# Optimization experiments

Measured on AMD Instinct MI355X. Metric: run time of the kernel, lower is better.

Reference implementation:

```python
import jax, jax.numpy as jnp
import numpy as np

B, NODES, IN_DIM, OUT_DIM, CAPS, K, NUM_ROUTE = 32, 512, 256, 128, 16, 5, 3

def squash(s):
    # s: [..., out]; scale = |s|^2/(1+|s|^2), direction s/(|s|+eps)
    sn = jnp.sum(s * s, axis=-1, keepdims=True)
    return (sn / (1.0 + sn)) * s / (jnp.sqrt(sn) + 1e-8)

def setup_inputs() -> dict:
    key = jax.random.key(0)
    k1, k2, k3, k4 = jax.random.split(key, 4)
    return {
        "x": jax.random.normal(k1, (B, NODES, IN_DIM), jnp.float32),
        "contribution": jax.random.normal(k2, (B, NODES), jnp.float32),
        "W": jax.random.normal(k3, (K, IN_DIM, OUT_DIM), jnp.float32),
        "alpha": jax.random.normal(k4, (NODES, CAPS, K), jnp.float32),
    }

def reference(x, contribution, W, alpha):
    # per-node, per-capsule transform: sum_k alpha[n,c,k] * W[k,i,o] -> [nodes, caps, in, out]
    Wn = jnp.einsum('nck,kio->ncio', alpha, W)
    # prediction vectors u_hat: [B, caps, nodes, out]
    u_hat = jnp.einsum('bni,ncio->bcno', x, Wn)
    u_det = jax.lax.stop_gradient(u_hat)
    # routing logits b init from (detached) contribution: [B, caps, nodes, 1]
    b = jnp.broadcast_to(
        jax.lax.stop_gradient(contribution)[:, None, :, None],
        (x.shape[0], CAPS, x.shape[1], 1))
    for _ in range(NUM_ROUTE):
        c = jax.nn.softmax(b, axis=1)              # over capsule axis
        v = squash(jnp.sum(c * u_det, axis=2))     # [B, caps, out]
        b = b + jnp.einsum('bcno,bco->bcn', u_det, v)[..., None]
    c = jax.nn.softmax(b, axis=1)
    s = jnp.sum(c * u_hat, axis=2)                 # [B, caps, out] (non-detached)
    return squash(s)
```

## Files before the change

kernel.cpp:

```cpp
#include <hip/hip_runtime.h>
#include <math.h>

#define B_ 32
#define NODES_ 512
#define IN_ 256
#define OUT_ 128
#define CAPS_ 16
#define KW_ 5
#define M_ (B_*NODES_)
#define N_ (KW_*OUT_)
#define NCH 32

typedef __attribute__((ext_vector_type(8))) short short8;
typedef __attribute__((ext_vector_type(4))) float f32x4;

#define Y_BOFF   0
#define L_BOFF   41943040
#define V_BOFF   42991616
#define SP_BOFF  43253760
#define BT_SZ    (N_*IN_*2)

__device__ __forceinline__ float b2f(unsigned short u) {
  union { unsigned int i; float f; } c; c.i = ((unsigned int)u) << 16; return c.f;
}

__device__ __forceinline__ unsigned short f2b(float f) {
  union { float f; unsigned int i; } c; c.f = f;
  unsigned int u = c.i;
  u += 0x7fffu + ((u >> 16) & 1u);
  return (unsigned short)(u >> 16);
}

__device__ __forceinline__ void async_load16(const void* g, void* l) {
  __builtin_amdgcn_global_load_lds(
      (const __attribute__((address_space(1))) unsigned int*)g,
      (__attribute__((address_space(3))) unsigned int*)l, 16, 0, 0);
}

__global__ __launch_bounds__(256) void conv_w(const float* __restrict__ W,
                                              unsigned short* __restrict__ bThi,
                                              unsigned short* __restrict__ bTlo) {
  int n = blockIdx.x;
  int i = threadIdx.x;
  int k = n >> 7, o = n & 127;
  float v = W[((size_t)k*IN_ + i)*OUT_ + o];
  unsigned short h = f2b(v);
  bThi[(size_t)n*IN_ + i] = h;
  bTlo[(size_t)n*IN_ + i] = f2b(v - b2f(h));
}

__global__ __launch_bounds__(256) void gemm_mfma(const float* __restrict__ x,
                                                 const unsigned short* __restrict__ bThi,
                                                 const unsigned short* __restrict__ bTlo,
                                                 float* __restrict__ y) {
  __shared__ float A_lds[8*128*4];
  __shared__ short Bh_lds[4*128*8];
  __shared__ short Bl_lds[4*128*8];
  const int t    = threadIdx.x;
  const int w    = t >> 6;
  const int lane = t & 63;
  const int wm   = w >> 1;
  const int wn   = w & 1;
  const int m0   = blockIdx.x * 128;
  const int n0   = blockIdx.y * 128;
  const int lrow = lane & 15;
  const int lk   = lane >> 4;

  f32x4 acc[4][4];
  #pragma unroll
  for (int i=0;i<4;++i)
    #pragma unroll
    for (int j=0;j<4;++j) acc[i][j] = (f32x4){0.f,0.f,0.f,0.f};

  for (int kb = 0; kb < IN_; kb += 32) {
    #pragma unroll
    for (int q=0; q<4; ++q) {
      int d0 = q*256 + w*64;
      int d  = d0 + lane;
      int cg = d >> 7;
      int r  = d & 127;
      async_load16(x + (size_t)(m0 + r)*IN_ + kb + cg*4, &A_lds[d0*4]);
    }
    #pragma unroll
    for (int q=0; q<2; ++q) {
      int d0 = q*256 + w*64;
      int d  = d0 + lane;
      int cg = d >> 7;
      int r  = d & 127;
      async_load16(bThi + (size_t)(n0 + r)*IN_ + kb + cg*8, &Bh_lds[d0*8]);
      async_load16(bTlo + (size_t)(n0 + r)*IN_ + kb + cg*8, &Bl_lds[d0*8]);
    }
    __syncthreads();

    short8 ah[4], al[4], bh[4], bl[4];
    #pragma unroll
    for (int mi=0; mi<4; ++mi) {
      int row_a = wm*64 + mi*16 + lrow;
      f32x4 a0 = *(const f32x4*)&A_lds[((2*lk  )*128 + row_a)*4];
      f32x4 a1 = *(const f32x4*)&A_lds[((2*lk+1)*128 + row_a)*4];
      #pragma unroll
      for (int j=0; j<8; ++j) {
        float f = (j < 4) ? a0[j] : a1[j-4];
        unsigned short h = f2b(f);
        ah[mi][j] = (short)h;
        al[mi][j] = (short)f2b(f - b2f(h));
      }
    }
    #pragma unroll
    for (int ni=0; ni<4; ++ni) {
      int row_b = wn*64 + ni*16 + lrow;
      bh[ni] = *(const short8*)&Bh_lds[(lk*128 + row_b)*8];
      bl[ni] = *(const short8*)&Bl_lds[(lk*128 + row_b)*8];
    }
    #pragma unroll
    for (int mi=0; mi<4; ++mi)
      #pragma unroll
      for (int ni=0; ni<4; ++ni) {
        acc[mi][ni] = __builtin_amdgcn_mfma_f32_16x16x32_bf16(bh[ni], ah[mi], acc[mi][ni], 0, 0, 0);
        acc[mi][ni] = __builtin_amdgcn_mfma_f32_16x16x32_bf16(bh[ni], al[mi], acc[mi][ni], 0, 0, 0);
        acc[mi][ni] = __builtin_amdgcn_mfma_f32_16x16x32_bf16(bl[ni], ah[mi], acc[mi][ni], 0, 0, 0);
      }
    __syncthreads();
  }

  #pragma unroll
  for (int mi=0; mi<4; ++mi) {
    int m = m0 + wm*64 + mi*16 + lrow;
    #pragma unroll
    for (int ni=0; ni<4; ++ni) {
      int nb = n0 + wn*64 + ni*16 + lk*4;
      float4 o = {acc[mi][ni][0], acc[mi][ni][1], acc[mi][ni][2], acc[mi][ni][3]};
      *(float4*)(y + (size_t)m*N_ + nb) = o;
    }
  }
}

__global__ __launch_bounds__(256) void route_step(const float* __restrict__ y,
                                                  const float* __restrict__ alpha,
                                                  const float* __restrict__ contrib,
                                                  float* __restrict__ logits,
                                                  const float* __restrict__ vin,
                                                  float* __restrict__ s_part,
                                                  int mode) {
  __shared__ __align__(16) float sh_y[16*644];
  __shared__ __align__(16) float sh_v[16*132];
  __shared__ __align__(16) float sh_alpha[16*16*5];
  __shared__ float sh_logit[16][16];
  __shared__ float sh_cw[16][16];

  const int t  = threadIdx.x;
  const int ch = blockIdx.x;
  const int b  = blockIdx.y;
  const int n0 = ch*16;

  const float* ybase = y + ((size_t)(b*NODES_ + n0))*KW_*OUT_;
  #pragma unroll
  for (int q=0; q<10; ++q) {
    int idx4 = t + q*256;
    int flat = idx4*4;
    int node = flat / 640;
    int rem  = flat - node*640;
    float4 vv = *(const float4*)(ybase + flat);
    *(float4*)&sh_y[node*644 + rem] = vv;
  }
  const float* abase = alpha + (size_t)n0*CAPS_*KW_;
  for (int i = t; i < 320; i += 256) {
    float4 av = *(const float4*)(abase + i*4);
    *(float4*)&sh_alpha[i*4] = av;
  }
  if (mode >= 1) {
    const float* vbase = vin + (size_t)b*CAPS_*OUT_;
    #pragma unroll
    for (int q=0; q<2; ++q) {
      int flat = (t + q*256)*4;
      int c = flat >> 7, o = flat & 127;
      float4 vv = *(const float4*)(vbase + flat);
      *(float4*)&sh_v[c*132 + o] = vv;
    }
    int node = t & 15, cap = t >> 4;
    sh_logit[node][cap] = logits[((size_t)b*CAPS_ + cap)*NODES_ + n0 + node];
  } else {
    int node = t & 15, cap = t >> 4;
    float cv = contrib[(size_t)b*NODES_ + n0 + node];
    sh_logit[node][cap] = cv;
    logits[((size_t)b*CAPS_ + cap)*NODES_ + n0 + node] = cv;
  }
  __syncthreads();

  if (mode >= 1) {
    int node = t >> 4, cap = t & 15;
    const float* al = &sh_alpha[(node*16+cap)*5];
    float a0=al[0],a1=al[1],a2=al[2],a3=al[3],a4=al[4];
    const float* yb = &sh_y[node*644];
    const float* vb = &sh_v[cap*132];
    float accd = 0.f;
    #pragma unroll 4
    for (int o=0; o<128; o+=4) {
      float4 y0 = *(const float4*)(yb + 0*128 + o);
      float4 y1 = *(const float4*)(yb + 1*128 + o);
      float4 y2 = *(const float4*)(yb + 2*128 + o);
      float4 y3 = *(const float4*)(yb + 3*128 + o);
      float4 y4 = *(const float4*)(yb + 4*128 + o);
      float4 vv = *(const float4*)(vb + o);
      float ux = a0*y0.x + a1*y1.x + a2*y2.x + a3*y3.x + a4*y4.x;
      float uy = a0*y0.y + a1*y1.y + a2*y2.y + a3*y3.y + a4*y4.y;
      float uz = a0*y0.z + a1*y1.z + a2*y2.z + a3*y3.z + a4*y4.z;
      float uw = a0*y0.w + a1*y1.w + a2*y2.w + a3*y3.w + a4*y4.w;
      accd += ux*vv.x + uy*vv.y + uz*vv.z + uw*vv.w;
    }
    float newl = sh_logit[node][cap] + accd;
    sh_logit[node][cap] = newl;
    logits[((size_t)b*CAPS_ + cap)*NODES_ + n0 + node] = newl;
    __syncthreads();
    if (t < 16) {
      int nd = t;
      float m = -1e30f;
      #pragma unroll
      for (int c=0;c<16;++c) m = fmaxf(m, sh_logit[nd][c]);
      float s = 0.f;
      float e[16];
      #pragma unroll
      for (int c=0;c<16;++c) { e[c] = __expf(sh_logit[nd][c]-m); s += e[c]; }
      float inv = 1.f/s;
      #pragma unroll
      for (int c=0;c<16;++c) sh_cw[nd][c] = e[c]*inv;
    }
  } else {
    int node = t >> 4, cap = t & 15;
    sh_cw[node][cap] = 1.f/16.f;
  }
  __syncthreads();

  float* spb = s_part + ((size_t)(b*NCH + ch))*CAPS_*OUT_;
  #pragma unroll
  for (int sl=0; sl<2; ++sl) {
    int slot = t + sl*256;
    int c = slot >> 5;
    int o = (slot & 31) * 4;
    float4 acc = {0.f,0.f,0.f,0.f};
    #pragma unroll 4
    for (int nd=0; nd<16; ++nd) {
      const float* al = &sh_alpha[(nd*16+c)*5];
      float a0=al[0],a1=al[1],a2=al[2],a3=al[3],a4=al[4];
      const float* yb = &sh_y[nd*644 + o];
      float4 y0 = *(const float4*)(yb);
      float4 y1 = *(const float4*)(yb + 128);
      float4 y2 = *(const float4*)(yb + 256);
      float4 y3 = *(const float4*)(yb + 384);
      float4 y4 = *(const float4*)(yb + 512);
      float cw = sh_cw[nd][c];
      acc.x += cw*(a0*y0.x + a1*y1.x + a2*y2.x + a3*y3.x + a4*y4.x);
      acc.y += cw*(a0*y0.y + a1*y1.y + a2*y2.y + a3*y3.y + a4*y4.y);
      acc.z += cw*(a0*y0.z + a1*y1.z + a2*y2.z + a3*y3.z + a4*y4.z);
      acc.w += cw*(a0*y0.w + a1*y1.w + a2*y2.w + a3*y3.w + a4*y4.w);
    }
    *(float4*)(spb + c*OUT_ + o) = acc;
  }
}

__global__ __launch_bounds__(128) void squash_k(const float* __restrict__ s_part,
                                                float* __restrict__ out) {
  const int bc = blockIdx.x;
  const int o  = threadIdx.x;
  const int b = bc >> 4, c = bc & 15;
  const float* sp = s_part + ((size_t)(b*NCH)*CAPS_ + c)*OUT_ + o;
  float s = 0.f;
  #pragma unroll
  for (int ch=0; ch<NCH; ++ch) s += sp[(size_t)ch*CAPS_*OUT_];
  float ss = s*s;
  #pragma unroll
  for (int off=32; off>0; off>>=1) ss += __shfl_down(ss, off, 64);
  __shared__ float red[2];
  if ((o & 63) == 0) red[o>>6] = ss;
  __syncthreads();
  float sn = red[0] + red[1];
  float scale = (sn/(1.f+sn)) / (sqrtf(sn)+1e-8f);
  out[(size_t)bc*OUT_ + o] = scale*s;
}

extern "C" void kernel_launch(void* const* d_in, const int* in_sizes, int n_in,
                              void* d_out, int out_size, void* d_ws, size_t ws_size,
                              hipStream_t stream) {
  const float* x       = (const float*)d_in[0];
  const float* contrib = (const float*)d_in[1];
  const float* W       = (const float*)d_in[2];
  const float* alpha   = (const float*)d_in[3];
  float* out = (float*)d_out;
  char*  wsb = (char*)d_ws;

  float* y             = (float*)(wsb + Y_BOFF);
  float* logits        = (float*)(wsb + L_BOFF);
  float* v             = (float*)(wsb + V_BOFF);
  float* s_part        = (float*)(wsb + SP_BOFF);
  unsigned short* bThi = (unsigned short*)(wsb + SP_BOFF);
  unsigned short* bTlo = (unsigned short*)(wsb + SP_BOFF + BT_SZ);

  conv_w<<<N_, 256, 0, stream>>>(W, bThi, bTlo);
  gemm_mfma<<<dim3(M_/128, N_/128), 256, 0, stream>>>(x, bThi, bTlo, y);

  route_step<<<dim3(NCH, B_), 256, 0, stream>>>(y, alpha, contrib, logits, v, s_part, 0);
  squash_k<<<B_*CAPS_, 128, 0, stream>>>(s_part, v);

  for (int it=0; it<3; ++it) {
    route_step<<<dim3(NCH, B_), 256, 0, stream>>>(y, alpha, contrib, logits, v, s_part, 1);
    squash_k<<<B_*CAPS_, 128, 0, stream>>>(s_part, (it==2) ? out : v);
  }
}
```

Baseline: 153.4 us.

## Pre-split x to bf16 hi/lo, use smaller GEMM tiles and 8-node routing chunks

Adds a conv_x pass that splits x into bf16 hi/lo arrays once, so the GEMM streams pre-split bf16 A tiles through async LDS loads instead of converting fp32 x inside the kernel. The GEMM tile shrinks to 64 rows with launch bounds asking for 4 blocks per CU, and the routing kernel handles 8 nodes per block across 64 chunks, giving more blocks and less LDS per block. The squash reduction is templated on the chunk count. The new path runs only when the workspace is large enough, otherwise the old path is kept. It costs an extra pass over x and twice as many partial sums to reduce.

Result: slower. 232.9 us (+51.8%).

```diff
diff --git a/kernel.cpp b/kernel.cpp
--- a/kernel.cpp
+++ b/kernel.cpp
@@ -9,7 +9,6 @@
 #define KW_ 5
 #define M_ (B_*NODES_)
 #define N_ (KW_*OUT_)
-#define NCH 32
 
 typedef __attribute__((ext_vector_type(8))) short short8;
 typedef __attribute__((ext_vector_type(4))) float f32x4;
@@ -19,22 +18,37 @@
 #define V_BOFF   42991616
 #define SP_BOFF  43253760
 #define BT_SZ    (N_*IN_*2)
+#define SP64_SZ  (B_*64*CAPS_*OUT_*4)
+#define WS_NEED_BIG (SP_BOFF + SP64_SZ)
+#define XSP_SZ   (M_*IN_*2)
 
 __device__ __forceinline__ float b2f(unsigned short u) {
   union { unsigned int i; float f; } c; c.i = ((unsigned int)u) << 16; return c.f;
 }
-
 __device__ __forceinline__ unsigned short f2b(float f) {
   union { float f; unsigned int i; } c; c.f = f;
   unsigned int u = c.i;
   u += 0x7fffu + ((u >> 16) & 1u);
   return (unsigned short)(u >> 16);
 }
-
 __device__ __forceinline__ void async_load16(const void* g, void* l) {
   __builtin_amdgcn_global_load_lds(
       (const __attribute__((address_space(1))) unsigned int*)g,
       (__attribute__((address_space(3))) unsigned int*)l, 16, 0, 0);
+}
+
+__global__ __launch_bounds__(256) void conv_x(const float* __restrict__ x,
+                                              unsigned short* __restrict__ xhi,
+                                              unsigned short* __restrict__ xlo) {
+  int idx = blockIdx.x*256 + threadIdx.x;
+  float4 v = *(const float4*)(x + (size_t)idx*4);
+  ushort4 h, l;
+  h.x = f2b(v.x); l.x = f2b(v.x - b2f(h.x));
+  h.y = f2b(v.y); l.y = f2b(v.y - b2f(h.y));
+  h.z = f2b(v.z); l.z = f2b(v.z - b2f(h.z));
+  h.w = f2b(v.w); l.w = f2b(v.w - b2f(h.w));
+  *(ushort4*)(xhi + (size_t)idx*4) = h;
+  *(ushort4*)(xlo + (size_t)idx*4) = l;
 }
 
 __global__ __launch_bounds__(256) void conv_w(const float* __restrict__ W,
@@ -49,10 +63,84 @@
   bTlo[(size_t)n*IN_ + i] = f2b(v - b2f(h));
 }
 
-__global__ __launch_bounds__(256) void gemm_mfma(const float* __restrict__ x,
-                                                 const unsigned short* __restrict__ bThi,
-                                                 const unsigned short* __restrict__ bTlo,
-                                                 float* __restrict__ y) {
+__global__ __launch_bounds__(256, 4) void gemm_bf4(const unsigned short* __restrict__ xhi,
+                                                   const unsigned short* __restrict__ xlo,
+                                                   const unsigned short* __restrict__ bThi,
+                                                   const unsigned short* __restrict__ bTlo,
+                                                   float* __restrict__ y) {
+  __shared__ short Ah_lds[4*64*8];
+  __shared__ short Al_lds[4*64*8];
+  __shared__ short Bh_lds[4*128*8];
+  __shared__ short Bl_lds[4*128*8];
+  const int t    = threadIdx.x;
+  const int lane = t & 63;
+  const int w    = t >> 6;
+  const int wm   = w >> 1;
+  const int wn   = w & 1;
+  const int m0   = blockIdx.x * 64;
+  const int n0   = blockIdx.y * 128;
+  const int lrow = lane & 15;
+  const int lk   = lane >> 4;
+
+  f32x4 acc[2][4];
+  #pragma unroll
+  for (int i=0;i<2;++i)
+    #pragma unroll
+    for (int j=0;j<4;++j) acc[i][j] = (f32x4){0.f,0.f,0.f,0.f};
+
+  const int cgA = t >> 6, rA = t & 63;
+  for (int kb = 0; kb < IN_; kb += 32) {
+    async_load16(xhi + (size_t)(m0 + rA)*IN_ + kb + cgA*8, &Ah_lds[t*8]);
+    async_load16(xlo + (size_t)(m0 + rA)*IN_ + kb + cgA*8, &Al_lds[t*8]);
+    #pragma unroll
+    for (int q=0; q<2; ++q) {
+      int d  = q*256 + t;
+      int cg = d >> 7, r = d & 127;
+      async_load16(bThi + (size_t)(n0 + r)*IN_ + kb + cg*8, &Bh_lds[d*8]);
+      async_load16(bTlo + (size_t)(n0 + r)*IN_ + kb + cg*8, &Bl_lds[d*8]);
+    }
+    __syncthreads();
+
+    short8 ah[2], al[2], bh[4], bl[4];
+    #pragma unroll
+    for (int mi=0; mi<2; ++mi) {
+      int row_a = wm*32 + mi*16 + lrow;
+      ah[mi] = *(const short8*)&Ah_lds[(lk*64 + row_a)*8];
+      al[mi] = *(const short8*)&Al_lds[(lk*64 + row_a)*8];
+    }
+    #pragma unroll
+    for (int ni=0; ni<4; ++ni) {
+      int row_b = wn*64 + ni*16 + lrow;
+      bh[ni] = *(const short8*)&Bh_lds[(lk*128 + row_b)*8];
+      bl[ni] = *(const short8*)&Bl_lds[(lk*128 + row_b)*8];
+    }
+    #pragma unroll
+    for (int mi=0; mi<2; ++mi)
+      #pragma unroll
+      for (int ni=0; ni<4; ++ni) {
+        acc[mi][ni] = __builtin_amdgcn_mfma_f32_16x16x32_bf16(bh[ni], ah[mi], acc[mi][ni], 0, 0, 0);
+        acc[mi][ni] = __builtin_amdgcn_mfma_f32_16x16x32_bf16(bh[ni], al[mi], acc[mi][ni], 0, 0, 0);
+        acc[mi][ni] = __builtin_amdgcn_mfma_f32_16x16x32_bf16(bl[ni], ah[mi], acc[mi][ni], 0, 0, 0);
+      }
+    __syncthreads();
+  }
+
+  #pragma unroll
+  for (int mi=0; mi<2; ++mi) {
+    int m = m0 + wm*32 + mi*16 + lrow;
+    #pragma unroll
+    for (int ni=0; ni<4; ++ni) {
+      int nb = n0 + wn*64 + ni*16 + lk*4;
+      float4 o = {acc[mi][ni][0], acc[mi][ni][1], acc[mi][ni][2], acc[mi][ni][3]};
+      *(float4*)(y + (size_t)m*N_ + nb) = o;
+    }
+  }
+}
+
+__global__ __launch_bounds__(256) void gemm_insplit(const float* __restrict__ x,
+                                                    const unsigned short* __restrict__ bThi,
+                                                    const unsigned short* __restrict__ bTlo,
+                                                    float* __restrict__ y) {
   __shared__ float A_lds[8*128*4];
   __shared__ short Bh_lds[4*128*8];
   __shared__ short Bl_lds[4*128*8];
@@ -135,13 +223,146 @@
   }
 }
 
-__global__ __launch_bounds__(256) void route_step(const float* __restrict__ y,
-                                                  const float* __restrict__ alpha,
-                                                  const float* __restrict__ contrib,
-                                                  float* __restrict__ logits,
-                                                  const float* __restrict__ vin,
-                                                  float* __restrict__ s_part,
-                                                  int mode) {
+__global__ __launch_bounds__(256) void route_step8(const float* __restrict__ y,
+                                                   const float* __restrict__ alpha,
+                                                   const float* __restrict__ contrib,
+                                                   float* __restrict__ logits,
+                                                   const float* __restrict__ vin,
+                                                   float* __restrict__ s_part,
+                                                   int mode) {
+  __shared__ __align__(16) float sh_y[8*644];
+  __shared__ __align__(16) float sh_v[16*132];
+  __shared__ __align__(16) float sh_alpha[8*16*5];
+  __shared__ float sh_logit[8][16];
+  __shared__ float sh_cw[8][16];
+
+  const int t  = threadIdx.x;
+  const int ch = blockIdx.x;
+  const int b  = blockIdx.y;
+  const int n0 = ch*8;
+
+  const float* ybase = y + ((size_t)(b*NODES_ + n0))*KW_*OUT_;
+  #pragma unroll
+  for (int q=0; q<5; ++q) {
+    int idx4 = t + q*256;
+    int flat = idx4*4;
+    int node = flat / 640;
+    int rem  = flat - node*640;
+    float4 vv = *(const float4*)(ybase + flat);
+    *(float4*)&sh_y[node*644 + rem] = vv;
+  }
+  const float* abase = alpha + (size_t)n0*CAPS_*KW_;
+  if (t < 160) {
+    float4 av = *(const float4*)(abase + t*4);
+    *(float4*)&sh_alpha[t*4] = av;
+  }
+  if (mode >= 1) {
+    const float* vbase = vin + (size_t)b*CAPS_*OUT_;
+    #pragma unroll
+    for (int q=0; q<2; ++q) {
+      int flat = (t + q*256)*4;
+      int c = flat >> 7, o = flat & 127;
+      float4 vv = *(const float4*)(vbase + flat);
+      *(float4*)&sh_v[c*132 + o] = vv;
+    }
+    if (t < 128) {
+      int node = t & 7, cap = t >> 3;
+      sh_logit[node][cap] = logits[((size_t)b*CAPS_ + cap)*NODES_ + n0 + node];
+    }
+  } else {
+    if (t < 128) {
+      int node = t & 7, cap = t >> 3;
+      float cv = contrib[(size_t)b*NODES_ + n0 + node];
+      sh_logit[node][cap] = cv;
+      logits[((size_t)b*CAPS_ + cap)*NODES_ + n0 + node] = cv;
+    }
+  }
+  __syncthreads();
+
+  if (mode >= 1) {
+    int node = t >> 5, cap = (t >> 1) & 15, half = t & 1;
+    const float* al = &sh_alpha[(node*16+cap)*5];
+    float a0=al[0],a1=al[1],a2=al[2],a3=al[3],a4=al[4];
+    const float* yb = &sh_y[node*644] + half*64;
+    const float* vb = &sh_v[cap*132]  + half*64;
+    float accd = 0.f;
+    #pragma unroll 4
+    for (int o=0; o<64; o+=4) {
+      float4 y0 = *(const float4*)(yb + 0*128 + o);
+      float4 y1 = *(const float4*)(yb + 1*128 + o);
+      float4 y2 = *(const float4*)(yb + 2*128 + o);
+      float4 y3 = *(const float4*)(yb + 3*128 + o);
+      float4 y4 = *(const float4*)(yb + 4*128 + o);
+      float4 vv = *(const float4*)(vb + o);
+      float ux = a0*y0.x + a1*y1.x + a2*y2.x + a3*y3.x + a4*y4.x;
+      float uy = a0*y0.y + a1*y1.y + a2*y2.y + a3*y3.y + a4*y4.y;
+      float uz = a0*y0.z + a1*y1.z + a2*y2.z + a3*y3.z + a4*y4.z;
+      float uw = a0*y0.w + a1*y1.w + a2*y2.w + a3*y3.w + a4*y4.w;
+      accd += ux*vv.x + uy*vv.y + uz*vv.z + uw*vv.w;
+    }
+    float tot = accd + __shfl_xor(accd, 1, 64);
+    if (half == 0) {
+      float newl = sh_logit[node][cap] + tot;
+      sh_logit[node][cap] = newl;
+      logits[((size_t)b*CAPS_ + cap)*NODES_ + n0 + node] = newl;
+    }
+    __syncthreads();
+    if (t < 8) {
+      int nd = t;
+      float m = -1e30f;
+      #pragma unroll
+      for (int c=0;c<16;++c) m = fmaxf(m, sh_logit[nd][c]);
+      float s = 0.f;
+      float e[16];
+      #pragma unroll
+      for (int c=0;c<16;++c) { e[c] = __expf(sh_logit[nd][c]-m); s += e[c]; }
+      float inv = 1.f/s;
+      #pragma unroll
+      for (int c=0;c<16;++c) sh_cw[nd][c] = e[c]*inv;
+    }
+  } else {
+    if (t < 128) sh_cw[t & 7][t >> 3] = 1.f/16.f;
+  }
+  __syncthreads();
+
+  {
+    int c  = t >> 4;
+    int o0 = (t & 15)*8;
+    float acc[8] = {0,0,0,0,0,0,0,0};
+    #pragma unroll 2
+    for (int nd=0; nd<8; ++nd) {
+      const float* al = &sh_alpha[(nd*16+c)*5];
+      float a0=al[0],a1=al[1],a2=al[2],a3=al[3],a4=al[4];
+      float cw = sh_cw[nd][c];
+      const float* yb = &sh_y[nd*644 + o0];
+      #pragma unroll
+      for (int h=0; h<2; ++h) {
+        float4 y0 = *(const float4*)(yb + h*4);
+        float4 y1 = *(const float4*)(yb + 128 + h*4);
+        float4 y2 = *(const float4*)(yb + 256 + h*4);
+        float4 y3 = *(const float4*)(yb + 384 + h*4);
+        float4 y4 = *(const float4*)(yb + 512 + h*4);
+        acc[h*4+0] += cw*(a0*y0.x + a1*y1.x + a2*y2.x + a3*y3.x + a4*y4.x);
+        acc[h*4+1] += cw*(a0*y0.y + a1*y1.y + a2*y2.y + a3*y3.y + a4*y4.y);
+        acc[h*4+2] += cw*(a0*y0.z + a1*y1.z + a2*y2.z + a3*y3.z + a4*y4.z);
+        acc[h*4+3] += cw*(a0*y0.w + a1*y1.w + a2*y2.w + a3*y3.w + a4*y4.w);
+      }
+    }
+    float* spb = s_part + ((size_t)(b*64 + ch)*CAPS_ + c)*OUT_ + o0;
+    float4 w0 = {acc[0],acc[1],acc[2],acc[3]};
+    float4 w1 = {acc[4],acc[5],acc[6],acc[7]};
+    *(float4*)(spb)     = w0;
+    *(float4*)(spb + 4) = w1;
+  }
+}
+
+__global__ __launch_bounds__(256) void route_step16(const float* __restrict__ y,
+                                                    const float* __restrict__ alpha,
+                                                    const float* __restrict__ contrib,
+                                                    float* __restrict__ logits,
+                                                    const float* __restrict__ vin,
+                                                    float* __restrict__ s_part,
+                                                    int mode) {
   __shared__ __align__(16) float sh_y[16*644];
   __shared__ __align__(16) float sh_v[16*132];
   __shared__ __align__(16) float sh_alpha[16*16*5];
@@ -231,7 +452,7 @@
   }
   __syncthreads();
 
-  float* spb = s_part + ((size_t)(b*NCH + ch))*CAPS_*OUT_;
+  float* spb = s_part + ((size_t)(b*32 + ch))*CAPS_*OUT_;
   #pragma unroll
   for (int sl=0; sl<2; ++sl) {
     int slot = t + sl*256;
@@ -258,15 +479,16 @@
   }
 }
 
+template<int NCHK>
 __global__ __launch_bounds__(128) void squash_k(const float* __restrict__ s_part,
                                                 float* __restrict__ out) {
   const int bc = blockIdx.x;
   const int o  = threadIdx.x;
   const int b = bc >> 4, c = bc & 15;
-  const float* sp = s_part + ((size_t)(b*NCH)*CAPS_ + c)*OUT_ + o;
+  const float* sp = s_part + ((size_t)(b*NCHK)*CAPS_ + c)*OUT_ + o;
   float s = 0.f;
   #pragma unroll
-  for (int ch=0; ch<NCH; ++ch) s += sp[(size_t)ch*CAPS_*OUT_];
+  for (int ch=0; ch<NCHK; ++ch) s += sp[(size_t)ch*CAPS_*OUT_];
   float ss = s*s;
   #pragma unroll
   for (int off=32; off>0; off>>=1) ss += __shfl_down(ss, off, 64);
@@ -288,21 +510,39 @@
   float* out = (float*)d_out;
   char*  wsb = (char*)d_ws;
 
-  float* y             = (float*)(wsb + Y_BOFF);
-  float* logits        = (float*)(wsb + L_BOFF);
-  float* v             = (float*)(wsb + V_BOFF);
-  float* s_part        = (float*)(wsb + SP_BOFF);
-  unsigned short* bThi = (unsigned short*)(wsb + SP_BOFF);
-  unsigned short* bTlo = (unsigned short*)(wsb + SP_BOFF + BT_SZ);
-
-  conv_w<<<N_, 256, 0, stream>>>(W, bThi, bTlo);
-  gemm_mfma<<<dim3(M_/128, N_/128), 256, 0, stream>>>(x, bThi, bTlo, y);
-
-  route_step<<<dim3(NCH, B_), 256, 0, stream>>>(y, alpha, contrib, logits, v, s_part, 0);
-  squash_k<<<B_*CAPS_, 128, 0, stream>>>(s_part, v);
-
-  for (int it=0; it<3; ++it) {
-    route_step<<<dim3(NCH, B_), 256, 0, stream>>>(y, alpha, contrib, logits, v, s_part, 1);
-    squash_k<<<B_*CAPS_, 128, 0, stream>>>(s_part, (it==2) ? out : v);
-  }
-}
+  float* y      = (float*)(wsb + Y_BOFF);
+  float* logits = (float*)(wsb + L_BOFF);
+  float* v      = (float*)(wsb + V_BOFF);
+  float* s_part = (float*)(wsb + SP_BOFF);
+
+  if (ws_size >= (size_t)WS_NEED_BIG) {
+    unsigned short* xhi  = (unsigned short*)(wsb + SP_BOFF);
+    unsigned short* xlo  = (unsigned short*)(wsb + SP_BOFF + XSP_SZ);
+    unsigned short* bThi = (unsigned short*)(wsb + L_BOFF);
+    unsigned short* bTlo = (unsigned short*)(wsb + L_BOFF + BT_SZ);
+
+    conv_x<<<4096, 256, 0, stream>>>(x, xhi, xlo);
+    conv_w<<<N_, 256, 0, stream>>>(W, bThi, bTlo);
+    gemm_bf4<<<dim3(M_/64, N_/128), 256, 0, stream>>>(xhi, xlo, bThi, bTlo, y);
+
+    route_step8<<<dim3(64, B_), 256, 0, stream>>>(y, alpha, contrib, logits, v, s_part, 0);
+    squash_k<64><<<B_*CAPS_, 128, 0, stream>>>(s_part, v);
+    for (int it=0; it<3; ++it) {
+      route_step8<<<dim3(64, B_), 256, 0, stream>>>(y, alpha, contrib, logits, v, s_part, 1);
+      squash_k<64><<<B_*CAPS_, 128, 0, stream>>>(s_part, (it==2) ? out : v);
+    }
+  } else {
+    unsigned short* bThi = (unsigned short*)(wsb + SP_BOFF);
+    unsigned short* bTlo = (unsigned short*)(wsb + SP_BOFF + BT_SZ);
+
+    conv_w<<<N_, 256, 0, stream>>>(W, bThi, bTlo);
+    gemm_insplit<<<dim3(M_/128, N_/128), 256, 0, stream>>>(x, bThi, bTlo, y);
+
+    route_step16<<<dim3(32, B_), 256, 0, stream>>>(y, alpha, contrib, logits, v, s_part, 0);
+    squash_k<32><<<B_*CAPS_, 128, 0, stream>>>(s_part, v);
+    for (int it=0; it<3; ++it) {
+      route_step16<<<dim3(32, B_), 256, 0, stream>>>(y, alpha, contrib, logits, v, s_part, 1);
+      squash_k<32><<<B_*CAPS_, 128, 0, stream>>>(s_part, (it==2) ? out : v);
+    }
+  }
+}
```

## Double-buffer GEMM LDS tiles and read routing v directly from global

Applied to the files above, without the earlier changes.

The GEMM kernel now double-buffers its A and B LDS tiles, issuing async global-to-LDS loads for the next K-block while MFMAs run on the current one, and fully unrolls the 8-step K loop. This is meant to hide global load latency behind compute, at the cost of twice the LDS per block, which may lower occupancy. Separately, route_step stops staging v into shared memory and reads it straight from global (cache), which removes a staging step and frees LDS but puts global loads in the inner dot-product loop.

Measured after the change: 172.5 us. 1.12x slower.

```diff
diff --git a/kernel.cpp b/kernel.cpp
--- a/kernel.cpp
+++ b/kernel.cpp
@@ -23,14 +23,12 @@
 __device__ __forceinline__ float b2f(unsigned short u) {
   union { unsigned int i; float f; } c; c.i = ((unsigned int)u) << 16; return c.f;
 }
-
 __device__ __forceinline__ unsigned short f2b(float f) {
   union { float f; unsigned int i; } c; c.f = f;
   unsigned int u = c.i;
   u += 0x7fffu + ((u >> 16) & 1u);
   return (unsigned short)(u >> 16);
 }
-
 __device__ __forceinline__ void async_load16(const void* g, void* l) {
   __builtin_amdgcn_global_load_lds(
       (const __attribute__((address_space(1))) unsigned int*)g,
@@ -49,13 +47,13 @@
   bTlo[(size_t)n*IN_ + i] = f2b(v - b2f(h));
 }
 
-__global__ __launch_bounds__(256) void gemm_mfma(const float* __restrict__ x,
+__global__ __launch_bounds__(256) void gemm_dbuf(const float* __restrict__ x,
                                                  const unsigned short* __restrict__ bThi,
                                                  const unsigned short* __restrict__ bTlo,
                                                  float* __restrict__ y) {
-  __shared__ float A_lds[8*128*4];
-  __shared__ short Bh_lds[4*128*8];
-  __shared__ short Bl_lds[4*128*8];
+  __shared__ float A_lds[2][8*128*4];
+  __shared__ short Bh_lds[2][4*128*8];
+  __shared__ short Bl_lds[2][4*128*8];
   const int t    = threadIdx.x;
   const int w    = t >> 6;
   const int lane = t & 63;
@@ -72,32 +70,40 @@
     #pragma unroll
     for (int j=0;j<4;++j) acc[i][j] = (f32x4){0.f,0.f,0.f,0.f};
 
-  for (int kb = 0; kb < IN_; kb += 32) {
-    #pragma unroll
-    for (int q=0; q<4; ++q) {
-      int d0 = q*256 + w*64;
-      int d  = d0 + lane;
-      int cg = d >> 7;
-      int r  = d & 127;
-      async_load16(x + (size_t)(m0 + r)*IN_ + kb + cg*4, &A_lds[d0*4]);
-    }
-    #pragma unroll
-    for (int q=0; q<2; ++q) {
-      int d0 = q*256 + w*64;
-      int d  = d0 + lane;
-      int cg = d >> 7;
-      int r  = d & 127;
-      async_load16(bThi + (size_t)(n0 + r)*IN_ + kb + cg*8, &Bh_lds[d0*8]);
-      async_load16(bTlo + (size_t)(n0 + r)*IN_ + kb + cg*8, &Bl_lds[d0*8]);
-    }
-    __syncthreads();
+#define STAGE_TILE(buf, kb) do {                                              \
+    _Pragma("unroll")                                                         \
+    for (int q=0; q<4; ++q) {                                                 \
+      int d0 = q*256 + w*64; int d = d0 + lane;                               \
+      int cg = d >> 7;  int r = d & 127;                                      \
+      async_load16(x + (size_t)(m0 + r)*IN_ + (kb) + cg*4, &A_lds[buf][d0*4]);\
+    }                                                                         \
+    _Pragma("unroll")                                                         \
+    for (int q=0; q<2; ++q) {                                                 \
+      int d0 = q*256 + w*64; int d = d0 + lane;                               \
+      int cg = d >> 7;  int r = d & 127;                                      \
+      async_load16(bThi + (size_t)(n0 + r)*IN_ + (kb) + cg*8, &Bh_lds[buf][d0*8]); \
+      async_load16(bTlo + (size_t)(n0 + r)*IN_ + (kb) + cg*8, &Bl_lds[buf][d0*8]); \
+    }                                                                         \
+  } while(0)
+
+  STAGE_TILE(0, 0);
+  __syncthreads();
+  int cur = 0;
+
+  #pragma unroll
+  for (int kbi = 0; kbi < 8; ++kbi) {
+    if (kbi < 7) STAGE_TILE(cur^1, (kbi+1)*32);
+
+    const float* Ac  = A_lds[cur];
+    const short* Bhc = Bh_lds[cur];
+    const short* Blc = Bl_lds[cur];
 
     short8 ah[4], al[4], bh[4], bl[4];
     #pragma unroll
     for (int mi=0; mi<4; ++mi) {
       int row_a = wm*64 + mi*16 + lrow;
-      f32x4 a0 = *(const f32x4*)&A_lds[((2*lk  )*128 + row_a)*4];
-      f32x4 a1 = *(const f32x4*)&A_lds[((2*lk+1)*128 + row_a)*4];
+      f32x4 a0 = *(const f32x4*)&Ac[((2*lk  )*128 + row_a)*4];
+      f32x4 a1 = *(const f32x4*)&Ac[((2*lk+1)*128 + row_a)*4];
       #pragma unroll
       for (int j=0; j<8; ++j) {
         float f = (j < 4) ? a0[j] : a1[j-4];
@@ -109,8 +115,8 @@
     #pragma unroll
     for (int ni=0; ni<4; ++ni) {
       int row_b = wn*64 + ni*16 + lrow;
-      bh[ni] = *(const short8*)&Bh_lds[(lk*128 + row_b)*8];
-      bl[ni] = *(const short8*)&Bl_lds[(lk*128 + row_b)*8];
+      bh[ni] = *(const short8*)&Bhc[(lk*128 + row_b)*8];
+      bl[ni] = *(const short8*)&Blc[(lk*128 + row_b)*8];
     }
     #pragma unroll
     for (int mi=0; mi<4; ++mi)
@@ -121,7 +127,9 @@
         acc[mi][ni] = __builtin_amdgcn_mfma_f32_16x16x32_bf16(bl[ni], ah[mi], acc[mi][ni], 0, 0, 0);
       }
     __syncthreads();
-  }
+    cur ^= 1;
+  }
+#undef STAGE_TILE
 
   #pragma unroll
   for (int mi=0; mi<4; ++mi) {
@@ -143,7 +151,6 @@
                                                   float* __restrict__ s_part,
                                                   int mode) {
   __shared__ __align__(16) float sh_y[16*644];
-  __shared__ __align__(16) float sh_v[16*132];
   __shared__ __align__(16) float sh_alpha[16*16*5];
   __shared__ float sh_logit[16][16];
   __shared__ float sh_cw[16][16];
@@ -168,22 +175,15 @@
     float4 av = *(const float4*)(abase + i*4);
     *(float4*)&sh_alpha[i*4] = av;
   }
-  if (mode >= 1) {
-    const float* vbase = vin + (size_t)b*CAPS_*OUT_;
-    #pragma unroll
-    for (int q=0; q<2; ++q) {
-      int flat = (t + q*256)*4;
-      int c = flat >> 7, o = flat & 127;
-      float4 vv = *(const float4*)(vbase + flat);
-      *(float4*)&sh_v[c*132 + o] = vv;
-    }
+  {
     int node = t & 15, cap = t >> 4;
-    sh_logit[node][cap] = logits[((size_t)b*CAPS_ + cap)*NODES_ + n0 + node];
-  } else {
-    int node = t & 15, cap = t >> 4;
-    float cv = contrib[(size_t)b*NODES_ + n0 + node];
-    sh_logit[node][cap] = cv;
-    logits[((size_t)b*CAPS_ + cap)*NODES_ + n0 + node] = cv;
+    if (mode >= 1) {
+      sh_logit[node][cap] = logits[((size_t)b*CAPS_ + cap)*NODES_ + n0 + node];
+    } else {
+      float cv = contrib[(size_t)b*NODES_ + n0 + node];
+      sh_logit[node][cap] = cv;
+      logits[((size_t)b*CAPS_ + cap)*NODES_ + n0 + node] = cv;
+    }
   }
   __syncthreads();
 
@@ -192,7 +192,7 @@
     const float* al = &sh_alpha[(node*16+cap)*5];
     float a0=al[0],a1=al[1],a2=al[2],a3=al[3],a4=al[4];
     const float* yb = &sh_y[node*644];
-    const float* vb = &sh_v[cap*132];
+    const float* vb = vin + (size_t)b*CAPS_*OUT_ + (size_t)cap*OUT_;
     float accd = 0.f;
     #pragma unroll 4
     for (int o=0; o<128; o+=4) {
@@ -296,7 +296,7 @@
   unsigned short* bTlo = (unsigned short*)(wsb + SP_BOFF + BT_SZ);
 
   conv_w<<<N_, 256, 0, stream>>>(W, bThi, bTlo);
-  gemm_mfma<<<dim3(M_/128, N_/128), 256, 0, stream>>>(x, bThi, bTlo, y);
+  gemm_dbuf<<<dim3(M_/128, N_/128), 256, 0, stream>>>(x, bThi, bTlo, y);
 
   route_step<<<dim3(NCH, B_), 256, 0, stream>>>(y, alpha, contrib, logits, v, s_part, 0);
   squash_k<<<B_*CAPS_, 128, 0, stream>>>(s_part, v);
```
